# Kernel tuning notes

Measured on AMD Instinct MI355X. Metric: run time of the kernel, lower is better.

## Reference

```python
import jax, jax.numpy as jnp
import numpy as np

EPS = 1e-7  # K.epsilon()
ROUTINGS = 3
NUM_CAPSULE = 8
FILTERS = 16


def squash(v, axis=-1):
    s2 = jnp.sum(jnp.square(v), axis=axis, keepdims=True)
    scale = s2 / (1.0 + s2) / jnp.sqrt(s2 + EPS)
    return scale * v


def _conv_per_caps(x, w):
    # x: [B,H,W,Cin], w: [k,k,Cin,Cout]
    return jax.lax.conv_general_dilated(
        x, w, window_strides=(1, 1), padding='SAME',
        dimension_numbers=('NHWC', 'HWIO', 'NHWC'))


def setup_inputs() -> dict:
    key = jax.random.key(0)
    k1, k2 = jax.random.split(key, 2)
    B, H, Wd, IN_CAPS, IN_F = 32, 32, 32, 8, 16
    input_tensor = jax.random.normal(k1, (B, H, Wd, IN_CAPS, IN_F), dtype=jnp.float32)
    # he_normal fan_in = k*k*Cin = 3*3*16 = 144
    W = jax.random.normal(k2, (IN_CAPS, 3, 3, IN_F, NUM_CAPSULE * FILTERS), dtype=jnp.float32) * np.sqrt(2.0 / 144.0)
    b = jnp.full((1, 1, NUM_CAPSULE, FILTERS), 0.1, dtype=jnp.float32)
    return {"input_tensor": input_tensor, "W": W, "b": b}


def reference(input_tensor, W, b):
    B, H, Wd, in_caps, in_f = input_tensor.shape
    # per-input-capsule conv: vmap over capsule axis of input and weight
    votes = jax.vmap(_conv_per_caps, in_axes=(3, 0), out_axes=1)(input_tensor, W)
    # [B, in_caps, H, W, num_cap*F] -> [B, in_caps, H, W, num_cap, F]
    votes = votes.reshape(B, in_caps, H, Wd, NUM_CAPSULE, FILTERS)

    # dynamic routing
    logits = jnp.zeros((B, in_caps, H, Wd, NUM_CAPSULE), dtype=votes.dtype)
    activation = None
    for i in range(ROUTINGS):
        route = jax.nn.softmax(logits, axis=-1)  # over output capsules
        # sum over input capsules of route-weighted votes, plus bias
        preactivate = jnp.einsum('bihwc,bihwcf->bhwcf', route, votes) + b
        activation = squash(preactivate, axis=-1)
        if i < ROUTINGS - 1:
            # scalar-product agreement
            logits = logits + jnp.einsum('bihwcf,bhwcf->bihwc', votes, activation)
    return activation.astype(jnp.float32)
```

## Files before the change

kernel.cpp:

```cpp
#include <hip/hip_runtime.h>
#include <math.h>


typedef _Float16 fp16x8 __attribute__((ext_vector_type(8)));
typedef float f32x4 __attribute__((ext_vector_type(4)));

#define EPS 1e-7f
constexpr int PSTRIDE = 136;
constexpr int PCOLS   = 34;
constexpr int LSTRIDE = 76;
constexpr int PXS     = 76;
constexpr int W_ELEMS = 40 * 8 * 64 * 8;

__device__ __forceinline__ float sumquad(float v) {
    v += __shfl_xor(v, 16);
    v += __shfl_xor(v, 32);
    return v;
}

__global__ __launch_bounds__(256)
void prep_weights(const float* __restrict__ wts,
                  _Float16* __restrict__ w16) {
    int n = blockIdx.x * 256 + threadIdx.x;
    if (n >= W_ELEMS) return;
    int j    = n & 7;
    int ln   = (n >> 3) & 63;
    int c0   = (n >> 9) & 7;
    int iq   = n >> 12;
    int i0   = iq / 5;
    int q0   = iq - i0 * 5;
    int k = q0 * 32 + (ln >> 4) * 8 + j;
    float w = 0.f;
    if (k < 144) w = wts[(i0 * 144 + k) * 128 + c0 * 16 + (ln & 15)];
    w16[n] = (_Float16)w;
}

__global__ __launch_bounds__(512, 4)
void capsule_mfma_kernel(const float* __restrict__ x,
                         const _Float16* __restrict__ w16,
                         const float* __restrict__ bias,
                         float* __restrict__ out)
{
    __shared__ _Float16 patch[3 * PCOLS * PSTRIDE];
    __shared__ float lg_arr[32 * LSTRIDE];
    __shared__ float r_arr[32 * PXS];

    const int tid  = threadIdx.x;
    const int lane = tid & 63;
    const int c    = tid >> 6;
    const int l15  = lane & 15;
    const int quad = lane >> 4;
    const int lane8 = lane * 8;

    const int bid = blockIdx.x;
    const int h = bid & 31, b = bid >> 5;

    const float4* x4 = (const float4*)x;
    for (int idx = tid; idx < 3 * PCOLS * 32; idx += 512) {
        int ch4  = idx & 31;
        int slot = idx >> 5;
        int row  = slot / PCOLS;
        int colp = slot - row * PCOLS;
        int gh = h - 1 + row;
        int gw = colp - 1;
        float4 v = {0.f, 0.f, 0.f, 0.f};
        if ((unsigned)gh < 32u && (unsigned)gw < 32u)
            v = x4[(((b * 32 + gh) * 32 + gw) << 5) + ch4];
        _Float16 ph[4];
        ph[0] = (_Float16)v.x; ph[1] = (_Float16)v.y;
        ph[2] = (_Float16)v.z; ph[3] = (_Float16)v.w;
        *(ushort4*)&patch[slot * PSTRIDE + ch4 * 4] = *(const ushort4*)ph;
    }
    __syncthreads();

    int a_off[5];
    #pragma unroll
    for (int q = 0; q < 5; ++q) {
        int tap = 2 * q + (quad >> 1);
        if (tap > 8) tap = 8;
        int dy = tap / 3, dx = tap - dy * 3;
        a_off[q] = (dy * PCOLS + l15 + dx) * PSTRIDE + (quad & 1) * 8;
    }

    f32x4 acc[2][8];
    #pragma unroll
    for (int mt = 0; mt < 2; ++mt)
        #pragma unroll
        for (int i = 0; i < 8; ++i) acc[mt][i] = (f32x4){0.f, 0.f, 0.f, 0.f};

    #pragma unroll
    for (int q = 0; q < 5; ++q) {
        #pragma unroll
        for (int i = 0; i < 8; ++i) {
            int woff = ((i * 5 + q) * 8 + c) * 512 + lane8;
            fp16x8 aw = *(const fp16x8*)(w16 + woff);
            fp16x8 b0 = *(const fp16x8*)(patch + a_off[q] + i * 16);
            fp16x8 b1 = *(const fp16x8*)(patch + a_off[q] + 16 * PSTRIDE + i * 16);
            acc[0][i] = __builtin_amdgcn_mfma_f32_16x16x32_f16(aw, b0, acc[0][i], 0, 0, 0);
            acc[1][i] = __builtin_amdgcn_mfma_f32_16x16x32_f16(aw, b1, acc[1][i], 0, 0, 0);
        }
    }

    const float4 bb4 = *(const float4*)(bias + c * 16 + quad * 4);
    const float barr[4] = {bb4.x, bb4.y, bb4.z, bb4.w};

    float actv[2][4];

    #pragma unroll
    for (int mt = 0; mt < 2; ++mt) {
        float pre[4];
        #pragma unroll
        for (int r = 0; r < 4; ++r) {
            float s = acc[mt][0][r] + acc[mt][1][r] + acc[mt][2][r] + acc[mt][3][r]
                    + acc[mt][4][r] + acc[mt][5][r] + acc[mt][6][r] + acc[mt][7][r];
            pre[r] = s * 0.125f + barr[r];
        }
        float s2 = sumquad(pre[0]*pre[0] + pre[1]*pre[1] + pre[2]*pre[2] + pre[3]*pre[3]);
        float scale = s2 * __builtin_amdgcn_rsqf(s2 + EPS) * __builtin_amdgcn_rcpf(1.f + s2);
        #pragma unroll
        for (int r = 0; r < 4; ++r) actv[mt][r] = scale * pre[r];
    }
    #pragma unroll
    for (int mt = 0; mt < 2; ++mt)
        #pragma unroll
        for (int i = 0; i < 8; ++i) {
            float t = acc[mt][i][0]*actv[mt][0] + acc[mt][i][1]*actv[mt][1]
                    + acc[mt][i][2]*actv[mt][2] + acc[mt][i][3]*actv[mt][3];
            t = sumquad(t);
            if (quad == 0) lg_arr[(mt * 16 + l15) * LSTRIDE + i * 9 + c] = t;
        }
    __syncthreads();
    if (tid < 256) {
        int p = tid >> 3, ii = tid & 7;
        const float* lrow = &lg_arr[p * LSTRIDE + ii * 9];
        float m = lrow[0];
        #pragma unroll
        for (int cc = 1; cc < 8; ++cc) m = fmaxf(m, lrow[cc]);
        float e[8]; float den = 0.f;
        #pragma unroll
        for (int cc = 0; cc < 8; ++cc) { e[cc] = __expf(lrow[cc] - m); den += e[cc]; }
        float rd = __builtin_amdgcn_rcpf(den);
        #pragma unroll
        for (int cc = 0; cc < 8; ++cc) r_arr[p * PXS + cc * 8 + ii] = e[cc] * rd;
    }
    __syncthreads();

    #pragma unroll
    for (int mt = 0; mt < 2; ++mt) {
        const float4* rp = (const float4*)&r_arr[(mt * 16 + l15) * PXS + c * 8];
        float4 r0 = rp[0], r1 = rp[1];
        float pre[4];
        #pragma unroll
        for (int r = 0; r < 4; ++r) {
            float s;
            s  = r0.x * acc[mt][0][r]; s = fmaf(r0.y, acc[mt][1][r], s);
            s  = fmaf(r0.z, acc[mt][2][r], s); s = fmaf(r0.w, acc[mt][3][r], s);
            s  = fmaf(r1.x, acc[mt][4][r], s); s = fmaf(r1.y, acc[mt][5][r], s);
            s  = fmaf(r1.z, acc[mt][6][r], s); s = fmaf(r1.w, acc[mt][7][r], s);
            pre[r] = s + barr[r];
        }
        float s2 = sumquad(pre[0]*pre[0] + pre[1]*pre[1] + pre[2]*pre[2] + pre[3]*pre[3]);
        float scale = s2 * __builtin_amdgcn_rsqf(s2 + EPS) * __builtin_amdgcn_rcpf(1.f + s2);
        #pragma unroll
        for (int r = 0; r < 4; ++r) actv[mt][r] = scale * pre[r];
    }
    #pragma unroll
    for (int mt = 0; mt < 2; ++mt)
        #pragma unroll
        for (int i = 0; i < 8; ++i) {
            float t = acc[mt][i][0]*actv[mt][0] + acc[mt][i][1]*actv[mt][1]
                    + acc[mt][i][2]*actv[mt][2] + acc[mt][i][3]*actv[mt][3];
            t = sumquad(t);
            if (quad == 0) lg_arr[(mt * 16 + l15) * LSTRIDE + i * 9 + c] += t;
        }
    __syncthreads();
    if (tid < 256) {
        int p = tid >> 3, ii = tid & 7;
        const float* lrow = &lg_arr[p * LSTRIDE + ii * 9];
        float m = lrow[0];
        #pragma unroll
        for (int cc = 1; cc < 8; ++cc) m = fmaxf(m, lrow[cc]);
        float e[8]; float den = 0.f;
        #pragma unroll
        for (int cc = 0; cc < 8; ++cc) { e[cc] = __expf(lrow[cc] - m); den += e[cc]; }
        float rd = __builtin_amdgcn_rcpf(den);
        #pragma unroll
        for (int cc = 0; cc < 8; ++cc) r_arr[p * PXS + cc * 8 + ii] = e[cc] * rd;
    }
    __syncthreads();

    #pragma unroll
    for (int mt = 0; mt < 2; ++mt) {
        const float4* rp = (const float4*)&r_arr[(mt * 16 + l15) * PXS + c * 8];
        float4 r0 = rp[0], r1 = rp[1];
        float pre[4];
        #pragma unroll
        for (int r = 0; r < 4; ++r) {
            float s;
            s  = r0.x * acc[mt][0][r]; s = fmaf(r0.y, acc[mt][1][r], s);
            s  = fmaf(r0.z, acc[mt][2][r], s); s = fmaf(r0.w, acc[mt][3][r], s);
            s  = fmaf(r1.x, acc[mt][4][r], s); s = fmaf(r1.y, acc[mt][5][r], s);
            s  = fmaf(r1.z, acc[mt][6][r], s); s = fmaf(r1.w, acc[mt][7][r], s);
            pre[r] = s + barr[r];
        }
        float s2 = sumquad(pre[0]*pre[0] + pre[1]*pre[1] + pre[2]*pre[2] + pre[3]*pre[3]);
        float scale = s2 * __builtin_amdgcn_rsqf(s2 + EPS) * __builtin_amdgcn_rcpf(1.f + s2);
        float4 o4 = { scale*pre[0], scale*pre[1], scale*pre[2], scale*pre[3] };
        int px = mt * 16 + l15;
        *(float4*)(out + (((b * 32 + h) * 32 + px) << 7) + c * 16 + quad * 4) = o4;
    }
}

extern "C" void kernel_launch(void* const* d_in, const int* in_sizes, int n_in,
                              void* d_out, int out_size, void* d_ws, size_t ws_size,
                              hipStream_t stream) {
    const float* x    = (const float*)d_in[0];
    const float* wts  = (const float*)d_in[1];
    const float* bias = (const float*)d_in[2];
    float* out        = (float*)d_out;
    _Float16* w16     = (_Float16*)d_ws;

    prep_weights<<<dim3(640), dim3(256), 0, stream>>>(wts, w16);
    capsule_mfma_kernel<<<dim3(1024), dim3(512), 0, stream>>>(x, w16, bias, out);
}
```

Baseline: 102.7 us.

## Process two output rows per block to reuse weight loads and patch halo

```diff
diff --git a/kernel.cpp b/kernel.cpp
--- a/kernel.cpp
+++ b/kernel.cpp
@@ -8,6 +8,7 @@
 #define EPS 1e-7f
 constexpr int PSTRIDE = 136;
 constexpr int PCOLS   = 34;
+constexpr int PROWS   = 4;
 constexpr int LSTRIDE = 76;
 constexpr int PXS     = 76;
 constexpr int W_ELEMS = 40 * 8 * 64 * 8;
@@ -35,15 +36,15 @@
     w16[n] = (_Float16)w;
 }
 
-__global__ __launch_bounds__(512, 4)
+__global__ __launch_bounds__(512, 2)
 void capsule_mfma_kernel(const float* __restrict__ x,
                          const _Float16* __restrict__ w16,
                          const float* __restrict__ bias,
                          float* __restrict__ out)
 {
-    __shared__ _Float16 patch[3 * PCOLS * PSTRIDE];
-    __shared__ float lg_arr[32 * LSTRIDE];
-    __shared__ float r_arr[32 * PXS];
+    __shared__ _Float16 patch[PROWS * PCOLS * PSTRIDE];
+    __shared__ float lg_arr[64 * LSTRIDE];
+    __shared__ float r_arr[64 * PXS];
 
     const int tid  = threadIdx.x;
     const int lane = tid & 63;
@@ -53,10 +54,11 @@
     const int lane8 = lane * 8;
 
     const int bid = blockIdx.x;
-    const int h = bid & 31, b = bid >> 5;
+    const int h2 = bid & 15, b = bid >> 4;
+    const int h = h2 << 1;
 
     const float4* x4 = (const float4*)x;
-    for (int idx = tid; idx < 3 * PCOLS * 32; idx += 512) {
+    for (int idx = tid; idx < PROWS * PCOLS * 32; idx += 512) {
         int ch4  = idx & 31;
         int slot = idx >> 5;
         int row  = slot / PCOLS;
@@ -82,9 +84,9 @@
         a_off[q] = (dy * PCOLS + l15 + dx) * PSTRIDE + (quad & 1) * 8;
     }
 
-    f32x4 acc[2][8];
-    #pragma unroll
-    for (int mt = 0; mt < 2; ++mt)
+    f32x4 acc[4][8];
+    #pragma unroll
+    for (int mt = 0; mt < 4; ++mt)
         #pragma unroll
         for (int i = 0; i < 8; ++i) acc[mt][i] = (f32x4){0.f, 0.f, 0.f, 0.f};
 
@@ -96,18 +98,22 @@
             fp16x8 aw = *(const fp16x8*)(w16 + woff);
             fp16x8 b0 = *(const fp16x8*)(patch + a_off[q] + i * 16);
             fp16x8 b1 = *(const fp16x8*)(patch + a_off[q] + 16 * PSTRIDE + i * 16);
+            fp16x8 b2 = *(const fp16x8*)(patch + a_off[q] + 34 * PSTRIDE + i * 16);
+            fp16x8 b3 = *(const fp16x8*)(patch + a_off[q] + 50 * PSTRIDE + i * 16);
             acc[0][i] = __builtin_amdgcn_mfma_f32_16x16x32_f16(aw, b0, acc[0][i], 0, 0, 0);
             acc[1][i] = __builtin_amdgcn_mfma_f32_16x16x32_f16(aw, b1, acc[1][i], 0, 0, 0);
+            acc[2][i] = __builtin_amdgcn_mfma_f32_16x16x32_f16(aw, b2, acc[2][i], 0, 0, 0);
+            acc[3][i] = __builtin_amdgcn_mfma_f32_16x16x32_f16(aw, b3, acc[3][i], 0, 0, 0);
         }
     }
 
     const float4 bb4 = *(const float4*)(bias + c * 16 + quad * 4);
     const float barr[4] = {bb4.x, bb4.y, bb4.z, bb4.w};
 
-    float actv[2][4];
-
-    #pragma unroll
-    for (int mt = 0; mt < 2; ++mt) {
+    float actv[4][4];
+
+    #pragma unroll
+    for (int mt = 0; mt < 4; ++mt) {
         float pre[4];
         #pragma unroll
         for (int r = 0; r < 4; ++r) {
@@ -121,16 +127,18 @@
         for (int r = 0; r < 4; ++r) actv[mt][r] = scale * pre[r];
     }
     #pragma unroll
-    for (int mt = 0; mt < 2; ++mt)
+    for (int mt = 0; mt < 4; ++mt) {
+        int pxid = (mt >> 1) * 32 + (mt & 1) * 16 + l15;
         #pragma unroll
         for (int i = 0; i < 8; ++i) {
             float t = acc[mt][i][0]*actv[mt][0] + acc[mt][i][1]*actv[mt][1]
                     + acc[mt][i][2]*actv[mt][2] + acc[mt][i][3]*actv[mt][3];
             t = sumquad(t);
-            if (quad == 0) lg_arr[(mt * 16 + l15) * LSTRIDE + i * 9 + c] = t;
-        }
-    __syncthreads();
-    if (tid < 256) {
+            if (quad == 0) lg_arr[pxid * LSTRIDE + i * 9 + c] = t;
+        }
+    }
+    __syncthreads();
+    {
         int p = tid >> 3, ii = tid & 7;
         const float* lrow = &lg_arr[p * LSTRIDE + ii * 9];
         float m = lrow[0];
@@ -146,8 +154,9 @@
     __syncthreads();
 
     #pragma unroll
-    for (int mt = 0; mt < 2; ++mt) {
-        const float4* rp = (const float4*)&r_arr[(mt * 16 + l15) * PXS + c * 8];
+    for (int mt = 0; mt < 4; ++mt) {
+        int pxid = (mt >> 1) * 32 + (mt & 1) * 16 + l15;
+        const float4* rp = (const float4*)&r_arr[pxid * PXS + c * 8];
         float4 r0 = rp[0], r1 = rp[1];
         float pre[4];
         #pragma unroll
@@ -165,16 +174,18 @@
         for (int r = 0; r < 4; ++r) actv[mt][r] = scale * pre[r];
     }
     #pragma unroll
-    for (int mt = 0; mt < 2; ++mt)
+    for (int mt = 0; mt < 4; ++mt) {
+        int pxid = (mt >> 1) * 32 + (mt & 1) * 16 + l15;
         #pragma unroll
         for (int i = 0; i < 8; ++i) {
             float t = acc[mt][i][0]*actv[mt][0] + acc[mt][i][1]*actv[mt][1]
                     + acc[mt][i][2]*actv[mt][2] + acc[mt][i][3]*actv[mt][3];
             t = sumquad(t);
-            if (quad == 0) lg_arr[(mt * 16 + l15) * LSTRIDE + i * 9 + c] += t;
-        }
-    __syncthreads();
-    if (tid < 256) {
+            if (quad == 0) lg_arr[pxid * LSTRIDE + i * 9 + c] += t;
+        }
+    }
+    __syncthreads();
+    {
         int p = tid >> 3, ii = tid & 7;
         const float* lrow = &lg_arr[p * LSTRIDE + ii * 9];
         float m = lrow[0];
@@ -190,8 +201,9 @@
     __syncthreads();
 
     #pragma unroll
-    for (int mt = 0; mt < 2; ++mt) {
-        const float4* rp = (const float4*)&r_arr[(mt * 16 + l15) * PXS + c * 8];
+    for (int mt = 0; mt < 4; ++mt) {
+        int pxid = (mt >> 1) * 32 + (mt & 1) * 16 + l15;
+        const float4* rp = (const float4*)&r_arr[pxid * PXS + c * 8];
         float4 r0 = rp[0], r1 = rp[1];
         float pre[4];
         #pragma unroll
@@ -206,8 +218,9 @@
         float s2 = sumquad(pre[0]*pre[0] + pre[1]*pre[1] + pre[2]*pre[2] + pre[3]*pre[3]);
         float scale = s2 * __builtin_amdgcn_rsqf(s2 + EPS) * __builtin_amdgcn_rcpf(1.f + s2);
         float4 o4 = { scale*pre[0], scale*pre[1], scale*pre[2], scale*pre[3] };
-        int px = mt * 16 + l15;
-        *(float4*)(out + (((b * 32 + h) * 32 + px) << 7) + c * 16 + quad * 4) = o4;
+        int gw = (mt & 1) * 16 + l15;
+        int gh = h + (mt >> 1);
+        *(float4*)(out + (((b * 32 + gh) * 32 + gw) << 7) + c * 16 + quad * 4) = o4;
     }
 }
 
@@ -221,5 +234,5 @@
     _Float16* w16     = (_Float16*)d_ws;
 
     prep_weights<<<dim3(640), dim3(256), 0, stream>>>(wts, w16);
-    capsule_mfma_kernel<<<dim3(1024), dim3(512), 0, stream>>>(x, w16, bias, out);
-}
+    capsule_mfma_kernel<<<dim3(512), dim3(512), 0, stream>>>(x, w16, bias, out);
+}
```

Result: slower. 107.9 us (+5.1%).

## Stream fp16 weight chunks into LDS with async global_load_lds ring buffer

Applied to the files above, without the earlier changes.

```diff
diff --git a/kernel.cpp b/kernel.cpp
--- a/kernel.cpp
+++ b/kernel.cpp
@@ -16,6 +16,12 @@
     v += __shfl_xor(v, 16);
     v += __shfl_xor(v, 32);
     return v;
+}
+
+__device__ __forceinline__ void gll16(const _Float16* g, _Float16* l) {
+    __builtin_amdgcn_global_load_lds(
+        (const __attribute__((address_space(1))) unsigned int*)(const void*)g,
+        (__attribute__((address_space(3))) unsigned int*)(void*)l, 16, 0, 0);
 }
 
 __global__ __launch_bounds__(256)
@@ -42,8 +48,10 @@
                          float* __restrict__ out)
 {
     __shared__ _Float16 patch[3 * PCOLS * PSTRIDE];
-    __shared__ float lg_arr[32 * LSTRIDE];
-    __shared__ float r_arr[32 * PXS];
+    __shared__ __align__(16) unsigned char smem_u[32768];
+    _Float16 (*Abuf)[8][512] = (_Float16 (*)[8][512])(void*)smem_u;
+    float* lg_arr = (float*)(void*)smem_u;
+    float* r_arr  = (float*)(void*)(smem_u + 9728);
 
     const int tid  = threadIdx.x;
     const int lane = tid & 63;
@@ -82,27 +90,38 @@
         a_off[q] = (dy * PCOLS + l15 + dx) * PSTRIDE + (quad & 1) * 8;
     }
 
-    f32x4 acc[2][8];
-    #pragma unroll
-    for (int mt = 0; mt < 2; ++mt)
-        #pragma unroll
-        for (int i = 0; i < 8; ++i) acc[mt][i] = (f32x4){0.f, 0.f, 0.f, 0.f};
-
-    #pragma unroll
-    for (int q = 0; q < 5; ++q) {
-        #pragma unroll
-        for (int i = 0; i < 8; ++i) {
-            int woff = ((i * 5 + q) * 8 + c) * 512 + lane8;
-            fp16x8 aw = *(const fp16x8*)(w16 + woff);
-            fp16x8 b0 = *(const fp16x8*)(patch + a_off[q] + i * 16);
-            fp16x8 b1 = *(const fp16x8*)(patch + a_off[q] + 16 * PSTRIDE + i * 16);
-            acc[0][i] = __builtin_amdgcn_mfma_f32_16x16x32_f16(aw, b0, acc[0][i], 0, 0, 0);
-            acc[1][i] = __builtin_amdgcn_mfma_f32_16x16x32_f16(aw, b1, acc[1][i], 0, 0, 0);
-        }
-    }
-
     const float4 bb4 = *(const float4*)(bias + c * 16 + quad * 4);
     const float barr[4] = {bb4.x, bb4.y, bb4.z, bb4.w};
+    asm volatile("s_waitcnt vmcnt(0)" ::: "memory");
+
+    const _Float16* gsrc = w16 + c * 512 + lane8;
+
+    gll16(gsrc + 0 * 4096, &Abuf[0][c][0]);
+    gll16(gsrc + 1 * 4096, &Abuf[1][c][0]);
+    gll16(gsrc + 2 * 4096, &Abuf[2][c][0]);
+
+    f32x4 acc[2][8];
+    #pragma unroll
+    for (int mt = 0; mt < 2; ++mt)
+        #pragma unroll
+        for (int i = 0; i < 8; ++i) acc[mt][i] = (f32x4){0.f, 0.f, 0.f, 0.f};
+
+    #pragma unroll
+    for (int ch = 0; ch < 40; ++ch) {
+        if (ch < 38)       asm volatile("s_waitcnt vmcnt(2)" ::: "memory");
+        else if (ch == 38) asm volatile("s_waitcnt vmcnt(1)" ::: "memory");
+        else               asm volatile("s_waitcnt vmcnt(0)" ::: "memory");
+        const int i = ch / 5;
+        const int q = ch - i * 5;
+        fp16x8 aw = *(const fp16x8*)&Abuf[ch & 3][c][lane8];
+        fp16x8 b0 = *(const fp16x8*)(patch + a_off[q] + i * 16);
+        fp16x8 b1 = *(const fp16x8*)(patch + a_off[q] + 16 * PSTRIDE + i * 16);
+        acc[0][i] = __builtin_amdgcn_mfma_f32_16x16x32_f16(aw, b0, acc[0][i], 0, 0, 0);
+        acc[1][i] = __builtin_amdgcn_mfma_f32_16x16x32_f16(aw, b1, acc[1][i], 0, 0, 0);
+        if (ch + 3 < 40)
+            gll16(gsrc + (ch + 3) * 4096, &Abuf[(ch + 3) & 3][c][0]);
+    }
+    __syncthreads();
 
     float actv[2][4];
 
```

New measurement: 105.3 us. 2.5% more time.

## Split each row block into two half-row blocks with two output capsules per wave

Applied to the files above, without the earlier changes.

```diff
diff --git a/kernel.cpp b/kernel.cpp
--- a/kernel.cpp
+++ b/kernel.cpp
@@ -7,7 +7,7 @@
 
 #define EPS 1e-7f
 constexpr int PSTRIDE = 136;
-constexpr int PCOLS   = 34;
+constexpr int PCOLS   = 18;
 constexpr int LSTRIDE = 76;
 constexpr int PXS     = 76;
 constexpr int W_ELEMS = 40 * 8 * 64 * 8;
@@ -35,34 +35,38 @@
     w16[n] = (_Float16)w;
 }
 
-__global__ __launch_bounds__(512, 4)
+__global__ __launch_bounds__(256, 4)
 void capsule_mfma_kernel(const float* __restrict__ x,
                          const _Float16* __restrict__ w16,
                          const float* __restrict__ bias,
                          float* __restrict__ out)
 {
     __shared__ _Float16 patch[3 * PCOLS * PSTRIDE];
-    __shared__ float lg_arr[32 * LSTRIDE];
-    __shared__ float r_arr[32 * PXS];
+    __shared__ float lg_arr[16 * LSTRIDE];
+    __shared__ float r_arr[16 * PXS];
 
     const int tid  = threadIdx.x;
     const int lane = tid & 63;
-    const int c    = tid >> 6;
+    const int w    = tid >> 6;
+    const int c0   = 2 * w;
     const int l15  = lane & 15;
     const int quad = lane >> 4;
     const int lane8 = lane * 8;
 
-    const int bid = blockIdx.x;
-    const int h = bid & 31, b = bid >> 5;
+    const int bid  = blockIdx.x;
+    const int half = bid & 1;
+    const int h    = (bid >> 1) & 31;
+    const int b    = bid >> 6;
+    const int pxbase = half * 16;
 
     const float4* x4 = (const float4*)x;
-    for (int idx = tid; idx < 3 * PCOLS * 32; idx += 512) {
+    for (int idx = tid; idx < 3 * PCOLS * 32; idx += 256) {
         int ch4  = idx & 31;
         int slot = idx >> 5;
         int row  = slot / PCOLS;
         int colp = slot - row * PCOLS;
         int gh = h - 1 + row;
-        int gw = colp - 1;
+        int gw = pxbase + colp - 1;
         float4 v = {0.f, 0.f, 0.f, 0.f};
         if ((unsigned)gh < 32u && (unsigned)gw < 32u)
             v = x4[(((b * 32 + gh) * 32 + gw) << 5) + ch4];
@@ -84,53 +88,57 @@
 
     f32x4 acc[2][8];
     #pragma unroll
-    for (int mt = 0; mt < 2; ++mt)
-        #pragma unroll
-        for (int i = 0; i < 8; ++i) acc[mt][i] = (f32x4){0.f, 0.f, 0.f, 0.f};
+    for (int cc = 0; cc < 2; ++cc)
+        #pragma unroll
+        for (int i = 0; i < 8; ++i) acc[cc][i] = (f32x4){0.f, 0.f, 0.f, 0.f};
 
     #pragma unroll
     for (int q = 0; q < 5; ++q) {
         #pragma unroll
         for (int i = 0; i < 8; ++i) {
-            int woff = ((i * 5 + q) * 8 + c) * 512 + lane8;
-            fp16x8 aw = *(const fp16x8*)(w16 + woff);
-            fp16x8 b0 = *(const fp16x8*)(patch + a_off[q] + i * 16);
-            fp16x8 b1 = *(const fp16x8*)(patch + a_off[q] + 16 * PSTRIDE + i * 16);
-            acc[0][i] = __builtin_amdgcn_mfma_f32_16x16x32_f16(aw, b0, acc[0][i], 0, 0, 0);
-            acc[1][i] = __builtin_amdgcn_mfma_f32_16x16x32_f16(aw, b1, acc[1][i], 0, 0, 0);
-        }
-    }
-
-    const float4 bb4 = *(const float4*)(bias + c * 16 + quad * 4);
-    const float barr[4] = {bb4.x, bb4.y, bb4.z, bb4.w};
+            int woff = ((i * 5 + q) * 8 + c0) * 512 + lane8;
+            fp16x8 a0 = *(const fp16x8*)(w16 + woff);
+            fp16x8 a1 = *(const fp16x8*)(w16 + woff + 512);
+            fp16x8 bb = *(const fp16x8*)(patch + a_off[q] + i * 16);
+            acc[0][i] = __builtin_amdgcn_mfma_f32_16x16x32_f16(a0, bb, acc[0][i], 0, 0, 0);
+            acc[1][i] = __builtin_amdgcn_mfma_f32_16x16x32_f16(a1, bb, acc[1][i], 0, 0, 0);
+        }
+    }
+
+    float barr[2][4];
+    #pragma unroll
+    for (int cc = 0; cc < 2; ++cc) {
+        float4 bb4 = *(const float4*)(bias + (c0 + cc) * 16 + quad * 4);
+        barr[cc][0] = bb4.x; barr[cc][1] = bb4.y; barr[cc][2] = bb4.z; barr[cc][3] = bb4.w;
+    }
 
     float actv[2][4];
 
     #pragma unroll
-    for (int mt = 0; mt < 2; ++mt) {
+    for (int cc = 0; cc < 2; ++cc) {
         float pre[4];
         #pragma unroll
         for (int r = 0; r < 4; ++r) {
-            float s = acc[mt][0][r] + acc[mt][1][r] + acc[mt][2][r] + acc[mt][3][r]
-                    + acc[mt][4][r] + acc[mt][5][r] + acc[mt][6][r] + acc[mt][7][r];
-            pre[r] = s * 0.125f + barr[r];
+            float s = acc[cc][0][r] + acc[cc][1][r] + acc[cc][2][r] + acc[cc][3][r]
+                    + acc[cc][4][r] + acc[cc][5][r] + acc[cc][6][r] + acc[cc][7][r];
+            pre[r] = s * 0.125f + barr[cc][r];
         }
         float s2 = sumquad(pre[0]*pre[0] + pre[1]*pre[1] + pre[2]*pre[2] + pre[3]*pre[3]);
         float scale = s2 * __builtin_amdgcn_rsqf(s2 + EPS) * __builtin_amdgcn_rcpf(1.f + s2);
         #pragma unroll
-        for (int r = 0; r < 4; ++r) actv[mt][r] = scale * pre[r];
-    }
-    #pragma unroll
-    for (int mt = 0; mt < 2; ++mt)
+        for (int r = 0; r < 4; ++r) actv[cc][r] = scale * pre[r];
+    }
+    #pragma unroll
+    for (int cc = 0; cc < 2; ++cc)
         #pragma unroll
         for (int i = 0; i < 8; ++i) {
-            float t = acc[mt][i][0]*actv[mt][0] + acc[mt][i][1]*actv[mt][1]
-                    + acc[mt][i][2]*actv[mt][2] + acc[mt][i][3]*actv[mt][3];
+            float t = acc[cc][i][0]*actv[cc][0] + acc[cc][i][1]*actv[cc][1]
+                    + acc[cc][i][2]*actv[cc][2] + acc[cc][i][3]*actv[cc][3];
             t = sumquad(t);
-            if (quad == 0) lg_arr[(mt * 16 + l15) * LSTRIDE + i * 9 + c] = t;
-        }
-    __syncthreads();
-    if (tid < 256) {
+            if (quad == 0) lg_arr[l15 * LSTRIDE + i * 9 + (c0 + cc)] = t;
+        }
+    __syncthreads();
+    if (tid < 128) {
         int p = tid >> 3, ii = tid & 7;
         const float* lrow = &lg_arr[p * LSTRIDE + ii * 9];
         float m = lrow[0];
@@ -146,35 +154,35 @@
     __syncthreads();
 
     #pragma unroll
-    for (int mt = 0; mt < 2; ++mt) {
-        const float4* rp = (const float4*)&r_arr[(mt * 16 + l15) * PXS + c * 8];
+    for (int cc = 0; cc < 2; ++cc) {
+        const float4* rp = (const float4*)&r_arr[l15 * PXS + (c0 + cc) * 8];
         float4 r0 = rp[0], r1 = rp[1];
         float pre[4];
         #pragma unroll
         for (int r = 0; r < 4; ++r) {
             float s;
-            s  = r0.x * acc[mt][0][r]; s = fmaf(r0.y, acc[mt][1][r], s);
-            s  = fmaf(r0.z, acc[mt][2][r], s); s = fmaf(r0.w, acc[mt][3][r], s);
-            s  = fmaf(r1.x, acc[mt][4][r], s); s = fmaf(r1.y, acc[mt][5][r], s);
-            s  = fmaf(r1.z, acc[mt][6][r], s); s = fmaf(r1.w, acc[mt][7][r], s);
-            pre[r] = s + barr[r];
+            s  = r0.x * acc[cc][0][r]; s = fmaf(r0.y, acc[cc][1][r], s);
+            s  = fmaf(r0.z, acc[cc][2][r], s); s = fmaf(r0.w, acc[cc][3][r], s);
+            s  = fmaf(r1.x, acc[cc][4][r], s); s = fmaf(r1.y, acc[cc][5][r], s);
+            s  = fmaf(r1.z, acc[cc][6][r], s); s = fmaf(r1.w, acc[cc][7][r], s);
+            pre[r] = s + barr[cc][r];
         }
         float s2 = sumquad(pre[0]*pre[0] + pre[1]*pre[1] + pre[2]*pre[2] + pre[3]*pre[3]);
         float scale = s2 * __builtin_amdgcn_rsqf(s2 + EPS) * __builtin_amdgcn_rcpf(1.f + s2);
         #pragma unroll
-        for (int r = 0; r < 4; ++r) actv[mt][r] = scale * pre[r];
-    }
-    #pragma unroll
-    for (int mt = 0; mt < 2; ++mt)
+        for (int r = 0; r < 4; ++r) actv[cc][r] = scale * pre[r];
+    }
+    #pragma unroll
+    for (int cc = 0; cc < 2; ++cc)
         #pragma unroll
         for (int i = 0; i < 8; ++i) {
-            float t = acc[mt][i][0]*actv[mt][0] + acc[mt][i][1]*actv[mt][1]
-                    + acc[mt][i][2]*actv[mt][2] + acc[mt][i][3]*actv[mt][3];
+            float t = acc[cc][i][0]*actv[cc][0] + acc[cc][i][1]*actv[cc][1]
+                    + acc[cc][i][2]*actv[cc][2] + acc[cc][i][3]*actv[cc][3];
             t = sumquad(t);
-            if (quad == 0) lg_arr[(mt * 16 + l15) * LSTRIDE + i * 9 + c] += t;
-        }
-    __syncthreads();
-    if (tid < 256) {
+            if (quad == 0) lg_arr[l15 * LSTRIDE + i * 9 + (c0 + cc)] += t;
+        }
+    __syncthreads();
+    if (tid < 128) {
         int p = tid >> 3, ii = tid & 7;
         const float* lrow = &lg_arr[p * LSTRIDE + ii * 9];
         float m = lrow[0];
@@ -190,24 +198,24 @@
     __syncthreads();
 
     #pragma unroll
-    for (int mt = 0; mt < 2; ++mt) {
-        const float4* rp = (const float4*)&r_arr[(mt * 16 + l15) * PXS + c * 8];
+    for (int cc = 0; cc < 2; ++cc) {
+        const float4* rp = (const float4*)&r_arr[l15 * PXS + (c0 + cc) * 8];
         float4 r0 = rp[0], r1 = rp[1];
         float pre[4];
         #pragma unroll
         for (int r = 0; r < 4; ++r) {
             float s;
-            s  = r0.x * acc[mt][0][r]; s = fmaf(r0.y, acc[mt][1][r], s);
-            s  = fmaf(r0.z, acc[mt][2][r], s); s = fmaf(r0.w, acc[mt][3][r], s);
-            s  = fmaf(r1.x, acc[mt][4][r], s); s = fmaf(r1.y, acc[mt][5][r], s);
-            s  = fmaf(r1.z, acc[mt][6][r], s); s = fmaf(r1.w, acc[mt][7][r], s);
-            pre[r] = s + barr[r];
+            s  = r0.x * acc[cc][0][r]; s = fmaf(r0.y, acc[cc][1][r], s);
+            s  = fmaf(r0.z, acc[cc][2][r], s); s = fmaf(r0.w, acc[cc][3][r], s);
+            s  = fmaf(r1.x, acc[cc][4][r], s); s = fmaf(r1.y, acc[cc][5][r], s);
+            s  = fmaf(r1.z, acc[cc][6][r], s); s = fmaf(r1.w, acc[cc][7][r], s);
+            pre[r] = s + barr[cc][r];
         }
         float s2 = sumquad(pre[0]*pre[0] + pre[1]*pre[1] + pre[2]*pre[2] + pre[3]*pre[3]);
         float scale = s2 * __builtin_amdgcn_rsqf(s2 + EPS) * __builtin_amdgcn_rcpf(1.f + s2);
         float4 o4 = { scale*pre[0], scale*pre[1], scale*pre[2], scale*pre[3] };
-        int px = mt * 16 + l15;
-        *(float4*)(out + (((b * 32 + h) * 32 + px) << 7) + c * 16 + quad * 4) = o4;
+        int px = pxbase + l15;
+        *(float4*)(out + (((b * 32 + h) * 32 + px) << 7) + (c0 + cc) * 16 + quad * 4) = o4;
     }
 }
 
@@ -221,5 +229,5 @@
     _Float16* w16     = (_Float16*)d_ws;
 
     prep_weights<<<dim3(640), dim3(256), 0, stream>>>(wts, w16);
-    capsule_mfma_kernel<<<dim3(1024), dim3(512), 0, stream>>>(x, w16, bias, out);
-}
+    capsule_mfma_kernel<<<dim3(2048), dim3(256), 0, stream>>>(x, w16, bias, out);
+}
```

Measured after the change: 107.7 us. +4.8%, slower.
